# Kernel optimization log

Hardware: AMD Instinct MI355X
Metric: run time of the kernel (lower is better)

Reference implementation:

```python
import jax, jax.numpy as jnp
import numpy as np

HEADS = 8
DIM_HEAD = 64
NUM_PATHWAYS = 281
SCALE = DIM_HEAD ** -0.5


def setup_inputs() -> dict:
    key = jax.random.key(0)
    k1, k2 = jax.random.split(key)
    b, n, dim = 4, 12281, 512  # n = 281 pathway tokens + 12000 histology patch tokens
    x = jax.random.normal(k1, (b, n, dim), dtype=jnp.float32)
    W_qkv = jax.random.normal(k2, (dim, 3 * HEADS * DIM_HEAD), dtype=jnp.float32) * 0.02
    return {"x": x, "W_qkv": W_qkv}


def reference(x, W_qkv):
    b, n, _ = x.shape
    h, d, m = HEADS, DIM_HEAD, NUM_PATHWAYS
    qkv = x @ W_qkv  # [b, n, 3*h*d]
    q, k, v = jnp.split(qkv, 3, axis=-1)
    # [b, n, h*d] -> [b, h, n, d]
    to_bhnd = lambda t: t.reshape(b, n, h, d).transpose(0, 2, 1, 3)
    q, k, v = to_bhnd(q), to_bhnd(k), to_bhnd(v)
    q = q * SCALE

    q_path, q_hist = q[:, :, :m], q[:, :, m:]
    k_path, k_hist = k[:, :, :m], k[:, :, m:]
    v_path, v_hist = v[:, :, :m], v[:, :, m:]

    # histology queries attend to pathway keys: [b, h, n_hist, m]
    attn_hist = jax.nn.softmax(jnp.einsum('bhid,bhjd->bhij', q_hist, k_path), axis=-1)
    # pathway queries attend to histology keys: [b, h, m, n_hist]
    attn_path = jax.nn.softmax(jnp.einsum('bhid,bhjd->bhij', q_path, k_hist), axis=-1)

    out_pathways = jnp.einsum('bhij,bhjd->bhid', attn_hist, v_path)   # [b, h, n_hist, d]
    out_histology = jnp.einsum('bhij,bhjd->bhid', attn_path, v_hist)  # [b, h, m, d]

    cross_token = jnp.concatenate([out_pathways, out_histology], axis=2)  # [b, h, n, d]
    return cross_token.transpose(0, 2, 1, 3).reshape(b, n, h * d)
```

## Files before the change

### kernel.cpp

```cpp
#include <hip/hip_runtime.h>
#include <hip/hip_bf16.h>

#define BATCH  4
#define NTOK   12281
#define DIMIN  512
#define HEADS  8
#define DHEAD  64
#define MPATH  281
#define NHIST  12000
#define QKVC   1536
#define QSCALE 0.125f
#define ROWS   (BATCH * NTOK)
#define MPAD   49152
#define NSPLIT 8
#define KSPL   1504
#define PROWS  320
#define HROWS  12032
#define M1B    576
#define M0B    3000

typedef __attribute__((ext_vector_type(8)))  short        short8v;
typedef __attribute__((ext_vector_type(4)))  float        f32x4;
typedef __attribute__((ext_vector_type(16))) float        f32x16;
typedef __attribute__((ext_vector_type(4)))  unsigned int uint4v;

__device__ __forceinline__ unsigned short f2bf(float f) {
    unsigned x = __builtin_bit_cast(unsigned, f);
    return (unsigned short)((x + 0x7fffu + ((x >> 16) & 1u)) >> 16);
}
__device__ __forceinline__ unsigned pk2(float a, float b) {
    return (unsigned)f2bf(a) | ((unsigned)f2bf(b) << 16);
}
__device__ __forceinline__ unsigned pk2n(float a, float b) {
    unsigned r;
    asm("v_cvt_pk_bf16_f32 %0, %1, %2" : "=v"(r) : "v"(a), "v"(b));
    return r;
}
__device__ __forceinline__ void plswap(unsigned &a, unsigned &b) {
    asm("v_permlane32_swap_b32 %0, %1" : "+v"(a), "+v"(b));
}
__device__ __forceinline__ short8v ld8(const unsigned short* p) {
    return *reinterpret_cast<const short8v*>(p);
}
__device__ __forceinline__ f32x16 MFMA32(short8v a, short8v b, f32x16 c) {
    return __builtin_amdgcn_mfma_f32_32x32x16_bf16(a, b, c, 0, 0, 0);
}
__device__ __forceinline__ void gl16(const char* g, char* l) {
    __builtin_amdgcn_global_load_lds(
        (const __attribute__((address_space(1))) unsigned int*)g,
        (__attribute__((address_space(3))) unsigned int*)l, 16, 0, 0);
}

__global__ __launch_bounds__(256)
void convert_x(const float* __restrict__ x, unsigned short* __restrict__ xb)
{
    size_t i = ((size_t)blockIdx.x * 256 + threadIdx.x) * 8;
    if (i >= (size_t)MPAD * DIMIN) return;
    uint4v o;
    if (i < (size_t)ROWS * DIMIN) {
        float4 a = *reinterpret_cast<const float4*>(x + i);
        float4 b = *reinterpret_cast<const float4*>(x + i + 4);
        o[0] = pk2(a.x, a.y); o[1] = pk2(a.z, a.w);
        o[2] = pk2(b.x, b.y); o[3] = pk2(b.z, b.w);
    } else {
        o[0] = o[1] = o[2] = o[3] = 0u;
    }
    *reinterpret_cast<uint4v*>(xb + i) = o;
}

__global__ __launch_bounds__(256)
void wt_convert(const float* __restrict__ w, unsigned short* __restrict__ wt)
{
    __shared__ unsigned short Ls[64][72];
    const int k0 = blockIdx.x * 64;
    const int n0 = blockIdx.y * 64;
    const int t  = threadIdx.x;
    const int lr = t >> 2;
    const int c0 = (t & 3) * 16;

    const float* sp = w + (size_t)(k0 + lr) * QKVC + n0 + c0;
    #pragma unroll
    for (int j = 0; j < 16; j += 4) {
        float4 a = *reinterpret_cast<const float4*>(sp + j);
        Ls[lr][c0 + j + 0] = f2bf(a.x);
        Ls[lr][c0 + j + 1] = f2bf(a.y);
        Ls[lr][c0 + j + 2] = f2bf(a.z);
        Ls[lr][c0 + j + 3] = f2bf(a.w);
    }
    __syncthreads();

    alignas(16) unsigned short tmp[16];
    #pragma unroll
    for (int j = 0; j < 16; ++j) tmp[j] = Ls[c0 + j][lr];
    unsigned short* dp = wt + (size_t)(n0 + lr) * DIMIN + k0 + c0;
    *reinterpret_cast<short8v*>(dp)     = *reinterpret_cast<short8v*>(&tmp[0]);
    *reinterpret_cast<short8v*>(dp + 8) = *reinterpret_cast<short8v*>(&tmp[8]);
}

__global__ __launch_bounds__(256)
void pad_fill(unsigned short* kpth, unsigned short* vpth,
              unsigned short* khst, unsigned short* vhst)
{
    int i = blockIdx.x * 256 + threadIdx.x;
    const int PPAD = (PROWS - MPATH) * DHEAD;
    const int HPAD = (HROWS - NHIST) * DHEAD;
    if (i < 32 * PPAD) {
        int bh = i / PPAD, r = i - bh * PPAD;
        size_t off = ((size_t)bh * PROWS + MPATH) * DHEAD + r;
        kpth[off] = 0; vpth[off] = 0;
    }
    if (i < 32 * HPAD) {
        int bh = i / HPAD, r = i - bh * HPAD;
        size_t off = ((size_t)bh * HROWS + NHIST) * DHEAD + r;
        khst[off] = 0; vhst[off] = 0;
    }
}

__global__ __launch_bounds__(256, 2)
void qkv_mfma(const unsigned short* __restrict__ xb, const unsigned short* __restrict__ wt,
              unsigned short* __restrict__ qb,
              unsigned short* __restrict__ kpth, unsigned short* __restrict__ khst,
              unsigned short* __restrict__ vpth, unsigned short* __restrict__ vhst)
{
    __shared__ char lds[65536];
    const int tid  = threadIdx.x;
    const int lane = tid & 63;
    const int wid  = tid >> 6;
    const int wr   = wid >> 1;
    const int wc   = wid & 1;

    int id  = blockIdx.x;
    int wg  = (id & 7) * 576 + (id >> 3);
    const int mt = wg / 12, nt = wg - mt * 12;
    const int bm = mt * 128, bn = nt * 128;

    const int arow0 = tid >> 3;
    const int acolS = ((tid & 7) << 4) ^ ((arow0 & 7) << 4);
    const char* xsrc = (const char*)xb + (((size_t)(bm + arow0)) << 10) + acolS;
    const char* wsrc = (const char*)wt + (((size_t)(bn + arow0)) << 10) + acolS;
    char* ldsA = lds + wid * 1024;
    char* ldsB = lds + 16384 + wid * 1024;

    const int rA   = wr * 64 + (lane & 15);
    const int rB   = wc * 64 + (lane & 15);
    const int hi16 = (lane >> 4) << 4;
    const int sxA  = (rA & 7) << 4;
    const int sxB  = (rB & 7) << 4;

    f32x4 acc[4][4];
    #pragma unroll
    for (int m = 0; m < 4; ++m)
        #pragma unroll
        for (int n = 0; n < 4; ++n)
            #pragma unroll
            for (int r = 0; r < 4; ++r) acc[m][n][r] = 0.f;

    auto STAGE = [&](int bufofs, int ks) {
        const char* xs = xsrc + (size_t)ks * 128;
        const char* ws = wsrc + (size_t)ks * 128;
        #pragma unroll
        for (int i = 0; i < 4; ++i)
            gl16(xs + ((size_t)i << 15), ldsA + bufofs + i * 4096);
        #pragma unroll
        for (int i = 0; i < 4; ++i)
            gl16(ws + ((size_t)i << 15), ldsB + bufofs + i * 4096);
    };

    STAGE(0, 0);
    asm volatile("s_waitcnt vmcnt(0)" ::: "memory");
    __syncthreads();

    for (int ks = 0; ks < 8; ++ks) {
        const int cur = ks & 1;
        if (ks < 7) STAGE((cur ^ 1) * 32768, ks + 1);

        const char* A = lds + cur * 32768;
        const char* B = A + 16384;
        #pragma unroll
        for (int kk = 0; kk < 2; ++kk) {
            short8v a[4], b[4];
            #pragma unroll
            for (int m = 0; m < 4; ++m)
                a[m] = *reinterpret_cast<const short8v*>(
                    A + (rA + m * 16) * 128 + ((kk * 64 + hi16) ^ sxA));
            #pragma unroll
            for (int n = 0; n < 4; ++n)
                b[n] = *reinterpret_cast<const short8v*>(
                    B + (rB + n * 16) * 128 + ((kk * 64 + hi16) ^ sxB));
            #pragma unroll
            for (int m = 0; m < 4; ++m)
                #pragma unroll
                for (int n = 0; n < 4; ++n)
                    acc[m][n] = __builtin_amdgcn_mfma_f32_16x16x32_bf16(
                        a[m], b[n], acc[m][n], 0, 0, 0);
        }
        asm volatile("s_waitcnt vmcnt(0)" ::: "memory");
        __syncthreads();
    }

    unsigned short* cl = reinterpret_cast<unsigned short*>(lds);
    const int crow0 = (lane >> 4) * 4;
    const int ccol  = lane & 15;
    #pragma unroll
    for (int n = 0; n < 4; ++n) {
        const int gcb = bn + wc * 64 + n * 16;
        const float scl = (gcb < 512) ? QSCALE : 1.f;
        #pragma unroll
        for (int m = 0; m < 4; ++m) {
            #pragma unroll
            for (int r = 0; r < 4; ++r) {
                int row = wr * 64 + m * 16 + crow0 + r;
                int col = wc * 64 + n * 16 + ccol;
                cl[row * 136 + col] = f2bf(acc[m][n][r] * scl);
            }
        }
    }
    __syncthreads();

    #pragma unroll
    for (int i = 0; i < 8; ++i) {
        const int chunk = tid + i * 256;
        const int row = chunk >> 4;
        const int c8  = (chunk & 15) * 8;
        const int grow = bm + row;
        if (grow < ROWS) {
            uint4v val = *reinterpret_cast<const uint4v*>(cl + row * 136 + c8);
            const int gcol  = bn + c8;
            const int which = gcol >> 9;
            const int rem   = gcol & 511;
            const int hh = rem >> 6, dd = rem & 63;
            const int bb = grow / NTOK;
            const int nn = grow - bb * NTOK;
            const int bh = bb * HEADS + hh;
            unsigned short* dst;
            if (which == 0) {
                dst = qb + ((size_t)bh * NTOK + nn) * DHEAD + dd;
            } else if (which == 1) {
                dst = (nn < MPATH) ? kpth + ((size_t)bh * PROWS + nn) * DHEAD + dd
                                   : khst + ((size_t)bh * HROWS + (nn - MPATH)) * DHEAD + dd;
            } else {
                dst = (nn < MPATH) ? vpth + ((size_t)bh * PROWS + nn) * DHEAD + dd
                                   : vhst + ((size_t)bh * HROWS + (nn - MPATH)) * DHEAD + dd;
            }
            *reinterpret_cast<uint4v*>(dst) = val;
        }
    }
}

__global__ __launch_bounds__(256)
void transpose64(const unsigned short* __restrict__ src, unsigned short* __restrict__ dst,
                 int nrpad)
{
    __shared__ unsigned short Ls[64][72];
    const int bh = blockIdx.y;
    const int r0 = blockIdx.x * 64;
    const unsigned short* s = src + (size_t)bh * nrpad * DHEAD;
    unsigned short*       d = dst + (size_t)bh * nrpad * DHEAD;

    const int t  = threadIdx.x;
    const int lr = t >> 2;
    const int c0 = (t & 3) * 16;

    const unsigned short* sp = s + (size_t)(r0 + lr) * DHEAD + c0;
    *reinterpret_cast<short8v*>(&Ls[lr][c0])     = *reinterpret_cast<const short8v*>(sp);
    *reinterpret_cast<short8v*>(&Ls[lr][c0 + 8]) = *reinterpret_cast<const short8v*>(sp + 8);
    __syncthreads();

    alignas(16) unsigned short tmp[16];
    #pragma unroll
    for (int j = 0; j < 16; ++j) tmp[j] = Ls[c0 + j][lr];
    const int T  = (r0 + c0) >> 5;
    const int kk = (r0 + c0) & 31;
    unsigned short* dp = d + (((size_t)T * 64 + lr) << 5) + kk;
    *reinterpret_cast<short8v*>(dp)     = *reinterpret_cast<short8v*>(&tmp[0]);
    *reinterpret_cast<short8v*>(dp + 8) = *reinterpret_cast<short8v*>(&tmp[8]);
}

__global__ __launch_bounds__(256, 4)
void fused_attn(const unsigned short* __restrict__ qb,
                const unsigned short* __restrict__ kpth, const unsigned short* __restrict__ khst,
                const unsigned short* __restrict__ vtp,  const unsigned short* __restrict__ vth,
                float* __restrict__ out,
                float* __restrict__ pl, float* __restrict__ po)
{
    const int wave = threadIdx.x >> 6;
    const int lane = threadIdx.x & 63;
    const int hi   = lane >> 5;
    const int ql   = lane & 31;

    int bh, qt, sp = 0;
    bool mode0;
    if (blockIdx.x < M1B) {
        mode0 = false;
        const int xcd = blockIdx.x & 7;
        const int i1  = (blockIdx.x >> 3) * 4 + wave;
        bh = i1 / 9;  qt = i1 - bh * 9;  sp = xcd;
    } else {
        mode0 = true;
        const int b0  = blockIdx.x - M1B;
        const int xcd = b0 & 7;
        const int i0  = (b0 >> 3) * 4 + wave;
        const int g   = i0 / 375;
        bh = xcd + 8 * g;  qt = i0 - g * 375;
    }

    const int q0 = mode0 ? (MPATH + qt * 32) : (qt * 32);
    const unsigned short* qrow = qb + ((size_t)bh * NTOK + (q0 + ql)) * DHEAD + hi * 8;
    short8v qf0 = ld8(qrow);
    short8v qf1 = ld8(qrow + 16);
    short8v qf2 = ld8(qrow + 32);
    short8v qf3 = ld8(qrow + 48);

    const unsigned short* kb;
    const unsigned short* vptr;
    int ntiles;
    if (mode0) {
        kb   = kpth + (size_t)bh * PROWS * DHEAD;
        vptr = vtp  + (size_t)bh * PROWS * DHEAD + ql * 32 + hi * 8;
        ntiles = 9;
    } else {
        kb   = khst + ((size_t)bh * HROWS + (size_t)sp * KSPL) * DHEAD;
        vptr = vth  + (size_t)bh * HROWS * DHEAD + (size_t)sp * 47 * 2048 + ql * 32 + hi * 8;
        ntiles = (sp == NSPLIT - 1) ? 46 : 47;
    }
    const unsigned short* kr = kb + (size_t)ql * DHEAD + hi * 8;

    f32x16 o0, o1;
    #pragma unroll
    for (int r = 0; r < 16; ++r) { o0[r] = 0.f; o1[r] = 0.f; }
    float l_loc = 0.f;

    short8v kf0 = ld8(kr);
    short8v kf1 = ld8(kr + 16);
    short8v kf2 = ld8(kr + 32);
    short8v kf3 = ld8(kr + 48);

    for (int t = 0; t < ntiles; ++t) {
        short8v vf0 = ld8(vptr);
        short8v vf1 = ld8(vptr + 16);
        short8v vf2 = ld8(vptr + 1024);
        short8v vf3 = ld8(vptr + 1024 + 16);
        vptr += 2048;

        f32x16 s;
        #pragma unroll
        for (int r = 0; r < 16; ++r) s[r] = 0.f;
        __builtin_amdgcn_s_setprio(1);
        s = MFMA32(kf0, qf0, s);
        s = MFMA32(kf1, qf1, s);
        s = MFMA32(kf2, qf2, s);
        s = MFMA32(kf3, qf3, s);
        __builtin_amdgcn_s_setprio(0);

        if (t + 1 < ntiles) {
            const unsigned short* kn = kr + (size_t)(t + 1) * 32 * DHEAD;
            kf0 = ld8(kn);
            kf1 = ld8(kn + 16);
            kf2 = ld8(kn + 32);
            kf3 = ld8(kn + 48);
        }

        float p[16]; float psum = 0.f;
        if (mode0 && t == 8) {
            #pragma unroll
            for (int r = 0; r < 16; ++r) {
                int krow = (r & 3) + 8 * (r >> 2) + 4 * hi;
                p[r] = (256 + krow >= MPATH) ? 0.f : __expf(s[r]);
                psum += p[r];
            }
        } else {
            #pragma unroll
            for (int r = 0; r < 16; ++r) { p[r] = __expf(s[r]); psum += p[r]; }
        }
        l_loc += psum;

        unsigned G[8];
        #pragma unroll
        for (int g = 0; g < 4; ++g) {
            G[2 * g]     = pk2n(p[4 * g],     p[4 * g + 1]);
            G[2 * g + 1] = pk2n(p[4 * g + 2], p[4 * g + 3]);
        }
        plswap(G[0], G[2]);
        plswap(G[1], G[3]);
        plswap(G[4], G[6]);
        plswap(G[5], G[7]);
        uint4v w0, w1;
        w0[0] = G[0]; w0[1] = G[1]; w0[2] = G[2]; w0[3] = G[3];
        w1[0] = G[4]; w1[1] = G[5]; w1[2] = G[6]; w1[3] = G[7];
        short8v pa0 = __builtin_bit_cast(short8v, w0);
        short8v pa1 = __builtin_bit_cast(short8v, w1);

        __builtin_amdgcn_s_setprio(1);
        o0 = MFMA32(pa0, vf0, o0);
        o0 = MFMA32(pa1, vf1, o0);
        o1 = MFMA32(pa0, vf2, o1);
        o1 = MFMA32(pa1, vf3, o1);
        __builtin_amdgcn_s_setprio(0);
    }

    const float l_run = l_loc + __shfl_xor(l_loc, 32);

    if (mode0) {
        const int bb = bh >> 3, hh = bh & 7;
        float linv = 1.0f / l_run;
        #pragma unroll
        for (int r = 0; r < 16; ++r) {
            int row = (r & 3) + 8 * (r >> 2) + 4 * hi;
            float invr = __shfl(linv, row);
            float* op = out + ((size_t)bb * NTOK + (qt * 32 + row)) * (HEADS * DHEAD) + hh * DHEAD;
            op[ql]      = o0[r] * invr;
            op[32 + ql] = o1[r] * invr;
        }
    } else {
        const size_t pbase = ((size_t)bh * NSPLIT + sp) * MPATH;
        if (hi == 0 && q0 + ql < MPATH)
            pl[pbase + q0 + ql] = l_run;
        #pragma unroll
        for (int r = 0; r < 16; ++r) {
            int row = (r & 3) + 8 * (r >> 2) + 4 * hi;
            int qq = q0 + row;
            if (qq < MPATH) {
                float* pp = po + (pbase + qq) * DHEAD;
                pp[ql]      = o0[r];
                pp[32 + ql] = o1[r];
            }
        }
    }
}

__global__ __launch_bounds__(256)
void combine_kernel(const float* __restrict__ pl, const float* __restrict__ po,
                    float* __restrict__ out)
{
    const int idx = blockIdx.x * 256 + threadIdx.x;
    const int dd  = idx & 63;
    const int r   = idx >> 6;
    if (r >= BATCH * HEADS * MPATH) return;
    const int bh = r / MPATH;
    const int jq = r - bh * MPATH;

    const size_t pbase = ((size_t)bh * NSPLIT) * MPATH + jq;
    float L = 0.f, acc = 0.f;
    #pragma unroll
    for (int s = 0; s < NSPLIT; ++s) {
        L   += pl[pbase + (size_t)s * MPATH];
        acc += po[(pbase + (size_t)s * MPATH) * DHEAD + dd];
    }
    const int bb = bh >> 3, hh = bh & 7;
    out[((size_t)bb * NTOK + (NHIST + jq)) * (HEADS * DHEAD) + hh * DHEAD + dd] = acc / L;
}

extern "C" void kernel_launch(void* const* d_in, const int* in_sizes, int n_in,
                              void* d_out, int out_size, void* d_ws, size_t ws_size,
                              hipStream_t stream)
{
    (void)in_sizes; (void)n_in; (void)out_size; (void)ws_size;
    const float* x = (const float*)d_in[0];
    const float* w = (const float*)d_in[1];
    float* out = (float*)d_out;

    const size_t QEL = (size_t)32 * NTOK * DHEAD;
    const size_t PEL = (size_t)32 * PROWS * DHEAD;
    const size_t HEL = (size_t)32 * HROWS * DHEAD;

    unsigned short* qb   = (unsigned short*)d_ws;
    unsigned short* kpth = qb   + QEL;
    unsigned short* khst = kpth + PEL;
    unsigned short* vpth = khst + HEL;
    unsigned short* vhst = vpth + PEL;
    unsigned short* vtp  = vhst + HEL;
    unsigned short* vth  = vtp  + PEL;
    unsigned short* xb   = vth  + HEL;
    unsigned short* wtb  = xb   + (size_t)MPAD * DIMIN;
    float* pl = (float*)(wtb + (size_t)QKVC * DIMIN);
    float* po = pl + (size_t)32 * NSPLIT * MPATH;

    convert_x<<<(MPAD * DIMIN / 8 + 255) / 256, 256, 0, stream>>>(x, xb);
    wt_convert<<<dim3(DIMIN / 64, QKVC / 64), 256, 0, stream>>>(w, wtb);
    pad_fill<<<312, 256, 0, stream>>>(kpth, vpth, khst, vhst);

    qkv_mfma<<<(MPAD / 128) * (QKVC / 128), 256, 0, stream>>>(xb, wtb, qb,
                                                              kpth, khst, vpth, vhst);

    transpose64<<<dim3(PROWS / 64, 32), 256, 0, stream>>>(vpth, vtp, PROWS);
    transpose64<<<dim3(HROWS / 64, 32), 256, 0, stream>>>(vhst, vth, HROWS);

    fused_attn<<<M1B + M0B, 256, 0, stream>>>(qb, kpth, khst, vtp, vth, out, pl, po);

    const int rows = BATCH * HEADS * MPATH;
    combine_kernel<<<(rows * DHEAD + 255) / 256, 256, 0, stream>>>(pl, po, out);
}
```

Measured before the change: 326.4 us.

## Software-pipeline QK^T one tile ahead and switch softmax to native exp2

The attention loop now computes the score MFMAs for tile t+1 before doing the exponentials and PV MFMAs for tile t, using two ping-pong score accumulators. K loads are prefetched two tiles ahead and V loads one tile ahead. The aim is to overlap the dependent MFMA, exp and pack chain across iterations and hide load latency. The exp is replaced by the hardware exp2, with log2(e) folded into the Q scale constant. This raises register pressure from the second 16-float accumulator and the extra in-flight fragments, which could reduce occupancy.

```diff
diff --git a/kernel.cpp b/kernel.cpp
--- a/kernel.cpp
+++ b/kernel.cpp
@@ -9,7 +9,7 @@
 #define MPATH  281
 #define NHIST  12000
 #define QKVC   1536
-#define QSCALE 0.125f
+#define QSCALE 0.180336884f
 #define ROWS   (BATCH * NTOK)
 #define MPAD   49152
 #define NSPLIT 8
@@ -38,6 +38,9 @@
 }
 __device__ __forceinline__ void plswap(unsigned &a, unsigned &b) {
     asm("v_permlane32_swap_b32 %0, %1" : "+v"(a), "+v"(b));
+}
+__device__ __forceinline__ float fexp2(float x) {
+    return __builtin_amdgcn_exp2f(x);
 }
 __device__ __forceinline__ short8v ld8(const unsigned short* p) {
     return *reinterpret_cast<const short8v*>(p);
@@ -311,19 +314,18 @@
     short8v qf2 = ld8(qrow + 32);
     short8v qf3 = ld8(qrow + 48);
 
-    const unsigned short* kb;
-    const unsigned short* vptr;
+    const unsigned short* kr;
+    const unsigned short* vb;
     int ntiles;
     if (mode0) {
-        kb   = kpth + (size_t)bh * PROWS * DHEAD;
-        vptr = vtp  + (size_t)bh * PROWS * DHEAD + ql * 32 + hi * 8;
+        kr = kpth + (size_t)bh * PROWS * DHEAD + ql * DHEAD + hi * 8;
+        vb = vtp  + (size_t)bh * PROWS * DHEAD + ql * 32 + hi * 8;
         ntiles = 9;
     } else {
-        kb   = khst + ((size_t)bh * HROWS + (size_t)sp * KSPL) * DHEAD;
-        vptr = vth  + (size_t)bh * HROWS * DHEAD + (size_t)sp * 47 * 2048 + ql * 32 + hi * 8;
+        kr = khst + ((size_t)bh * HROWS + (size_t)sp * KSPL) * DHEAD + ql * DHEAD + hi * 8;
+        vb = vth  + (size_t)bh * HROWS * DHEAD + (size_t)sp * 47 * 2048 + ql * 32 + hi * 8;
         ntiles = (sp == NSPLIT - 1) ? 46 : 47;
     }
-    const unsigned short* kr = kb + (size_t)ql * DHEAD + hi * 8;
 
     f32x16 o0, o1;
     #pragma unroll
@@ -334,51 +336,64 @@
     short8v kf1 = ld8(kr + 16);
     short8v kf2 = ld8(kr + 32);
     short8v kf3 = ld8(kr + 48);
-
-    for (int t = 0; t < ntiles; ++t) {
-        short8v vf0 = ld8(vptr);
-        short8v vf1 = ld8(vptr + 16);
-        short8v vf2 = ld8(vptr + 1024);
-        short8v vf3 = ld8(vptr + 1024 + 16);
-        vptr += 2048;
-
-        f32x16 s;
-        #pragma unroll
-        for (int r = 0; r < 16; ++r) s[r] = 0.f;
-        __builtin_amdgcn_s_setprio(1);
-        s = MFMA32(kf0, qf0, s);
-        s = MFMA32(kf1, qf1, s);
-        s = MFMA32(kf2, qf2, s);
-        s = MFMA32(kf3, qf3, s);
-        __builtin_amdgcn_s_setprio(0);
-
-        if (t + 1 < ntiles) {
-            const unsigned short* kn = kr + (size_t)(t + 1) * 32 * DHEAD;
-            kf0 = ld8(kn);
-            kf1 = ld8(kn + 16);
-            kf2 = ld8(kn + 32);
-            kf3 = ld8(kn + 48);
-        }
-
-        float p[16]; float psum = 0.f;
+    short8v vf0 = ld8(vb);
+    short8v vf1 = ld8(vb + 16);
+    short8v vf2 = ld8(vb + 1024);
+    short8v vf3 = ld8(vb + 1040);
+
+    f32x16 sA, sB;
+    #pragma unroll
+    for (int r = 0; r < 16; ++r) sA[r] = 0.f;
+    sA = MFMA32(kf0, qf0, sA);
+    sA = MFMA32(kf1, qf1, sA);
+    sA = MFMA32(kf2, qf2, sA);
+    sA = MFMA32(kf3, qf3, sA);
+    kf0 = ld8(kr + 2048);
+    kf1 = ld8(kr + 2048 + 16);
+    kf2 = ld8(kr + 2048 + 32);
+    kf3 = ld8(kr + 2048 + 48);
+
+    auto body = [&](f32x16& scur, f32x16& snxt, int t) {
+        const bool hn = (t + 1 < ntiles);
+        if (hn) {
+            #pragma unroll
+            for (int r = 0; r < 16; ++r) snxt[r] = 0.f;
+            __builtin_amdgcn_s_setprio(1);
+            snxt = MFMA32(kf0, qf0, snxt);
+            snxt = MFMA32(kf1, qf1, snxt);
+            snxt = MFMA32(kf2, qf2, snxt);
+            snxt = MFMA32(kf3, qf3, snxt);
+            __builtin_amdgcn_s_setprio(0);
+            if (t + 2 < ntiles) {
+                const unsigned short* kn = kr + (size_t)(t + 2) * 2048;
+                kf0 = ld8(kn);
+                kf1 = ld8(kn + 16);
+                kf2 = ld8(kn + 32);
+                kf3 = ld8(kn + 48);
+            }
+        }
+        float psum = 0.f;
         if (mode0 && t == 8) {
             #pragma unroll
             for (int r = 0; r < 16; ++r) {
                 int krow = (r & 3) + 8 * (r >> 2) + 4 * hi;
-                p[r] = (256 + krow >= MPATH) ? 0.f : __expf(s[r]);
-                psum += p[r];
+                float e = (256 + krow >= MPATH) ? 0.f : fexp2(scur[r]);
+                scur[r] = e; psum += e;
             }
         } else {
             #pragma unroll
-            for (int r = 0; r < 16; ++r) { p[r] = __expf(s[r]); psum += p[r]; }
+            for (int r = 0; r < 16; ++r) {
+                float e = fexp2(scur[r]);
+                scur[r] = e; psum += e;
+            }
         }
         l_loc += psum;
 
         unsigned G[8];
         #pragma unroll
         for (int g = 0; g < 4; ++g) {
-            G[2 * g]     = pk2n(p[4 * g],     p[4 * g + 1]);
-            G[2 * g + 1] = pk2n(p[4 * g + 2], p[4 * g + 3]);
+            G[2 * g]     = pk2n(scur[4 * g],     scur[4 * g + 1]);
+            G[2 * g + 1] = pk2n(scur[4 * g + 2], scur[4 * g + 3]);
         }
         plswap(G[0], G[2]);
         plswap(G[1], G[3]);
@@ -396,6 +411,21 @@
         o1 = MFMA32(pa0, vf2, o1);
         o1 = MFMA32(pa1, vf3, o1);
         __builtin_amdgcn_s_setprio(0);
+
+        if (hn) {
+            const unsigned short* vn = vb + (size_t)(t + 1) * 2048;
+            vf0 = ld8(vn);
+            vf1 = ld8(vn + 16);
+            vf2 = ld8(vn + 1024);
+            vf3 = ld8(vn + 1040);
+        }
+    };
+
+    for (int t = 0;;) {
+        body(sA, sB, t);
+        if (++t >= ntiles) break;
+        body(sB, sA, t);
+        if (++t >= ntiles) break;
     }
 
     const float l_run = l_loc + __shfl_xor(l_loc, 32);
```

Measured after the change: 594.1 us. 82.0% more time.

## Process two query tiles per wave, use exp2 with folded log2e scale, split keys 16 ways

Applied to the files above, without the earlier changes.

Each wave now handles 64 queries (two 32-row tiles) and reuses every loaded K and V fragment across both, which halves K/V load traffic per query. The Q scale folds in log2(e) so the softmax can call the hardware exp2 directly instead of __expf. The histology-key split grows from 8 to 16 chunks, with new grid sizes, and the launch bound drops to 2 blocks per SIMD to leave room for the extra accumulators. The Q buffer gets padding so the over-read of the last tile stays in bounds. Costs include higher register pressure, lower occupancy, more partial results for the combine step, and some idle waves (pw>=5 return early).

```diff
diff --git a/kernel.cpp b/kernel.cpp
--- a/kernel.cpp
+++ b/kernel.cpp
@@ -9,15 +9,16 @@
 #define MPATH  281
 #define NHIST  12000
 #define QKVC   1536
-#define QSCALE 0.125f
+#define QSCALE 0.180336884f
 #define ROWS   (BATCH * NTOK)
 #define MPAD   49152
-#define NSPLIT 8
-#define KSPL   1504
+#define NSPLIT 16
+#define KSPL   768
 #define PROWS  320
 #define HROWS  12032
-#define M1B    576
-#define M0B    3000
+#define M1B    1024
+#define M0B    1504
+#define QPAD   4096
 
 typedef __attribute__((ext_vector_type(8)))  short        short8v;
 typedef __attribute__((ext_vector_type(4)))  float        f32x4;
@@ -38,6 +39,9 @@
 }
 __device__ __forceinline__ void plswap(unsigned &a, unsigned &b) {
     asm("v_permlane32_swap_b32 %0, %1" : "+v"(a), "+v"(b));
+}
+__device__ __forceinline__ float fexp2(float x) {
+    return __builtin_amdgcn_exp2f(x);
 }
 __device__ __forceinline__ short8v ld8(const unsigned short* p) {
     return *reinterpret_cast<const short8v*>(p);
@@ -276,8 +280,8 @@
     *reinterpret_cast<short8v*>(dp + 8) = *reinterpret_cast<short8v*>(&tmp[8]);
 }
 
-__global__ __launch_bounds__(256, 4)
-void fused_attn(const unsigned short* __restrict__ qb,
+__global__ __launch_bounds__(256, 2)
+void fused_attn(const unsigned short* __restrict__ qbuf,
                 const unsigned short* __restrict__ kpth, const unsigned short* __restrict__ khst,
                 const unsigned short* __restrict__ vtp,  const unsigned short* __restrict__ vth,
                 float* __restrict__ out,
@@ -288,141 +292,175 @@
     const int hi   = lane >> 5;
     const int ql   = lane & 31;
 
-    int bh, qt, sp = 0;
+    int bh, pw, sp = 0;
     bool mode0;
     if (blockIdx.x < M1B) {
         mode0 = false;
         const int xcd = blockIdx.x & 7;
-        const int i1  = (blockIdx.x >> 3) * 4 + wave;
-        bh = i1 / 9;  qt = i1 - bh * 9;  sp = xcd;
+        const int jj  = blockIdx.x >> 3;
+        bh = jj >> 2;
+        const int rem = jj & 3;
+        sp = xcd + 8 * (rem & 1);
+        pw = (rem >> 1) * 4 + wave;
+        if (pw >= 5) return;
     } else {
         mode0 = true;
         const int b0  = blockIdx.x - M1B;
         const int xcd = b0 & 7;
-        const int i0  = (b0 >> 3) * 4 + wave;
-        const int g   = i0 / 375;
-        bh = xcd + 8 * g;  qt = i0 - g * 375;
-    }
-
-    const int q0 = mode0 ? (MPATH + qt * 32) : (qt * 32);
-    const unsigned short* qrow = qb + ((size_t)bh * NTOK + (q0 + ql)) * DHEAD + hi * 8;
-    short8v qf0 = ld8(qrow);
-    short8v qf1 = ld8(qrow + 16);
-    short8v qf2 = ld8(qrow + 32);
-    short8v qf3 = ld8(qrow + 48);
-
-    const unsigned short* kb;
-    const unsigned short* vptr;
+        const int i   = b0 >> 3;
+        const int g   = i / 47;
+        bh = xcd + 8 * g;
+        pw = (i - g * 47) * 4 + wave;
+    }
+
+    const int q0 = mode0 ? (MPATH + pw * 64) : (pw * 64);
+    const unsigned short* qra = qbuf + ((size_t)bh * NTOK + (q0 + ql)) * DHEAD + hi * 8;
+    const unsigned short* qrb = qra + (size_t)32 * DHEAD;
+    short8v qA0 = ld8(qra),      qA1 = ld8(qra + 16);
+    short8v qA2 = ld8(qra + 32), qA3 = ld8(qra + 48);
+    short8v qB0 = ld8(qrb),      qB1 = ld8(qrb + 16);
+    short8v qB2 = ld8(qrb + 32), qB3 = ld8(qrb + 48);
+
+    const unsigned short* kr;
+    const unsigned short* vb;
     int ntiles;
     if (mode0) {
-        kb   = kpth + (size_t)bh * PROWS * DHEAD;
-        vptr = vtp  + (size_t)bh * PROWS * DHEAD + ql * 32 + hi * 8;
+        kr = kpth + (size_t)bh * PROWS * DHEAD + ql * DHEAD + hi * 8;
+        vb = vtp  + (size_t)bh * PROWS * DHEAD + ql * 32 + hi * 8;
         ntiles = 9;
     } else {
-        kb   = khst + ((size_t)bh * HROWS + (size_t)sp * KSPL) * DHEAD;
-        vptr = vth  + (size_t)bh * HROWS * DHEAD + (size_t)sp * 47 * 2048 + ql * 32 + hi * 8;
-        ntiles = (sp == NSPLIT - 1) ? 46 : 47;
-    }
-    const unsigned short* kr = kb + (size_t)ql * DHEAD + hi * 8;
-
-    f32x16 o0, o1;
-    #pragma unroll
-    for (int r = 0; r < 16; ++r) { o0[r] = 0.f; o1[r] = 0.f; }
-    float l_loc = 0.f;
-
-    short8v kf0 = ld8(kr);
-    short8v kf1 = ld8(kr + 16);
-    short8v kf2 = ld8(kr + 32);
-    short8v kf3 = ld8(kr + 48);
+        kr = khst + ((size_t)bh * HROWS + (size_t)sp * KSPL) * DHEAD + ql * DHEAD + hi * 8;
+        vb = vth  + (size_t)bh * HROWS * DHEAD + (size_t)sp * 24 * 2048 + ql * 32 + hi * 8;
+        ntiles = (sp == NSPLIT - 1) ? 15 : 24;
+    }
+
+    f32x16 o0, o1, o2, o3, SZ;
+    #pragma unroll
+    for (int r = 0; r < 16; ++r) { o0[r] = 0.f; o1[r] = 0.f; o2[r] = 0.f; o3[r] = 0.f; SZ[r] = 0.f; }
+    float lA = 0.f, lB = 0.f;
+
+    short8v kf0 = ld8(kr), kf1 = ld8(kr + 16), kf2 = ld8(kr + 32), kf3 = ld8(kr + 48);
 
     for (int t = 0; t < ntiles; ++t) {
-        short8v vf0 = ld8(vptr);
-        short8v vf1 = ld8(vptr + 16);
-        short8v vf2 = ld8(vptr + 1024);
-        short8v vf3 = ld8(vptr + 1024 + 16);
-        vptr += 2048;
-
-        f32x16 s;
-        #pragma unroll
-        for (int r = 0; r < 16; ++r) s[r] = 0.f;
+        const unsigned short* vp = vb + (size_t)t * 2048;
+        short8v vf0 = ld8(vp);
+        short8v vf1 = ld8(vp + 16);
+        short8v vf2 = ld8(vp + 1024);
+        short8v vf3 = ld8(vp + 1040);
+
         __builtin_amdgcn_s_setprio(1);
-        s = MFMA32(kf0, qf0, s);
-        s = MFMA32(kf1, qf1, s);
-        s = MFMA32(kf2, qf2, s);
-        s = MFMA32(kf3, qf3, s);
+        f32x16 sA = MFMA32(kf0, qA0, SZ);
+        sA = MFMA32(kf1, qA1, sA);
+        sA = MFMA32(kf2, qA2, sA);
+        sA = MFMA32(kf3, qA3, sA);
+        f32x16 sB = MFMA32(kf0, qB0, SZ);
+        sB = MFMA32(kf1, qB1, sB);
+        sB = MFMA32(kf2, qB2, sB);
+        sB = MFMA32(kf3, qB3, sB);
         __builtin_amdgcn_s_setprio(0);
 
         if (t + 1 < ntiles) {
-            const unsigned short* kn = kr + (size_t)(t + 1) * 32 * DHEAD;
-            kf0 = ld8(kn);
-            kf1 = ld8(kn + 16);
-            kf2 = ld8(kn + 32);
-            kf3 = ld8(kn + 48);
-        }
-
-        float p[16]; float psum = 0.f;
+            const unsigned short* kn = kr + (size_t)(t + 1) * 2048;
+            kf0 = ld8(kn);      kf1 = ld8(kn + 16);
+            kf2 = ld8(kn + 32); kf3 = ld8(kn + 48);
+        }
+
+        float psA = 0.f, psB = 0.f;
         if (mode0 && t == 8) {
             #pragma unroll
             for (int r = 0; r < 16; ++r) {
                 int krow = (r & 3) + 8 * (r >> 2) + 4 * hi;
-                p[r] = (256 + krow >= MPATH) ? 0.f : __expf(s[r]);
-                psum += p[r];
+                float eA = (256 + krow >= MPATH) ? 0.f : fexp2(sA[r]);
+                float eB = (256 + krow >= MPATH) ? 0.f : fexp2(sB[r]);
+                sA[r] = eA; psA += eA;
+                sB[r] = eB; psB += eB;
             }
         } else {
             #pragma unroll
-            for (int r = 0; r < 16; ++r) { p[r] = __expf(s[r]); psum += p[r]; }
-        }
-        l_loc += psum;
-
-        unsigned G[8];
-        #pragma unroll
-        for (int g = 0; g < 4; ++g) {
-            G[2 * g]     = pk2n(p[4 * g],     p[4 * g + 1]);
-            G[2 * g + 1] = pk2n(p[4 * g + 2], p[4 * g + 3]);
-        }
-        plswap(G[0], G[2]);
-        plswap(G[1], G[3]);
-        plswap(G[4], G[6]);
-        plswap(G[5], G[7]);
-        uint4v w0, w1;
-        w0[0] = G[0]; w0[1] = G[1]; w0[2] = G[2]; w0[3] = G[3];
-        w1[0] = G[4]; w1[1] = G[5]; w1[2] = G[6]; w1[3] = G[7];
-        short8v pa0 = __builtin_bit_cast(short8v, w0);
-        short8v pa1 = __builtin_bit_cast(short8v, w1);
+            for (int r = 0; r < 16; ++r) {
+                float eA = fexp2(sA[r]); sA[r] = eA; psA += eA;
+                float eB = fexp2(sB[r]); sB[r] = eB; psB += eB;
+            }
+        }
+        lA += psA; lB += psB;
+
+        unsigned A0 = pk2n(sA[0],  sA[1]),  A1 = pk2n(sA[2],  sA[3]);
+        unsigned A2 = pk2n(sA[4],  sA[5]),  A3 = pk2n(sA[6],  sA[7]);
+        unsigned A4 = pk2n(sA[8],  sA[9]),  A5 = pk2n(sA[10], sA[11]);
+        unsigned A6 = pk2n(sA[12], sA[13]), A7 = pk2n(sA[14], sA[15]);
+        plswap(A0, A2); plswap(A1, A3); plswap(A4, A6); plswap(A5, A7);
+        uint4v wA0, wA1;
+        wA0[0] = A0; wA0[1] = A1; wA0[2] = A2; wA0[3] = A3;
+        wA1[0] = A4; wA1[1] = A5; wA1[2] = A6; wA1[3] = A7;
+        short8v paA0 = __builtin_bit_cast(short8v, wA0);
+        short8v paA1 = __builtin_bit_cast(short8v, wA1);
+        unsigned B0 = pk2n(sB[0],  sB[1]),  B1 = pk2n(sB[2],  sB[3]);
+        unsigned B2 = pk2n(sB[4],  sB[5]),  B3 = pk2n(sB[6],  sB[7]);
+        unsigned B4 = pk2n(sB[8],  sB[9]),  B5 = pk2n(sB[10], sB[11]);
+        unsigned B6 = pk2n(sB[12], sB[13]), B7 = pk2n(sB[14], sB[15]);
+        plswap(B0, B2); plswap(B1, B3); plswap(B4, B6); plswap(B5, B7);
+        uint4v wB0, wB1;
+        wB0[0] = B0; wB0[1] = B1; wB0[2] = B2; wB0[3] = B3;
+        wB1[0] = B4; wB1[1] = B5; wB1[2] = B6; wB1[3] = B7;
+        short8v paB0 = __builtin_bit_cast(short8v, wB0);
+        short8v paB1 = __builtin_bit_cast(short8v, wB1);
 
         __builtin_amdgcn_s_setprio(1);
-        o0 = MFMA32(pa0, vf0, o0);
-        o0 = MFMA32(pa1, vf1, o0);
-        o1 = MFMA32(pa0, vf2, o1);
-        o1 = MFMA32(pa1, vf3, o1);
+        o0 = MFMA32(paA0, vf0, o0);
+        o0 = MFMA32(paA1, vf1, o0);
+        o1 = MFMA32(paA0, vf2, o1);
+        o1 = MFMA32(paA1, vf3, o1);
+        o2 = MFMA32(paB0, vf0, o2);
+        o2 = MFMA32(paB1, vf1, o2);
+        o3 = MFMA32(paB0, vf2, o3);
+        o3 = MFMA32(paB1, vf3, o3);
         __builtin_amdgcn_s_setprio(0);
     }
 
-    const float l_run = l_loc + __shfl_xor(l_loc, 32);
+    const float lAr = lA + __shfl_xor(lA, 32);
+    const float lBr = lB + __shfl_xor(lB, 32);
 
     if (mode0) {
         const int bb = bh >> 3, hh = bh & 7;
-        float linv = 1.0f / l_run;
+        const float liA = 1.0f / lAr;
+        const float liB = 1.0f / lBr;
         #pragma unroll
         for (int r = 0; r < 16; ++r) {
-            int row = (r & 3) + 8 * (r >> 2) + 4 * hi;
-            float invr = __shfl(linv, row);
-            float* op = out + ((size_t)bb * NTOK + (qt * 32 + row)) * (HEADS * DHEAD) + hh * DHEAD;
-            op[ql]      = o0[r] * invr;
-            op[32 + ql] = o1[r] * invr;
+            const int row = (r & 3) + 8 * (r >> 2) + 4 * hi;
+            {
+                float invr = __shfl(liA, row);
+                float* op = out + ((size_t)bb * NTOK + (pw * 64 + row)) * (HEADS * DHEAD) + hh * DHEAD;
+                op[ql]      = o0[r] * invr;
+                op[32 + ql] = o1[r] * invr;
+            }
+            const int tokB = pw * 64 + 32 + row;
+            if (tokB < NHIST) {
+                float invr = __shfl(liB, row);
+                float* op = out + ((size_t)bb * NTOK + tokB) * (HEADS * DHEAD) + hh * DHEAD;
+                op[ql]      = o2[r] * invr;
+                op[32 + ql] = o3[r] * invr;
+            }
         }
     } else {
         const size_t pbase = ((size_t)bh * NSPLIT + sp) * MPATH;
-        if (hi == 0 && q0 + ql < MPATH)
-            pl[pbase + q0 + ql] = l_run;
+        if (hi == 0) {
+            if (q0 + ql < MPATH)      pl[pbase + q0 + ql]      = lAr;
+            if (q0 + 32 + ql < MPATH) pl[pbase + q0 + 32 + ql] = lBr;
+        }
         #pragma unroll
         for (int r = 0; r < 16; ++r) {
-            int row = (r & 3) + 8 * (r >> 2) + 4 * hi;
-            int qq = q0 + row;
-            if (qq < MPATH) {
-                float* pp = po + (pbase + qq) * DHEAD;
+            const int row = (r & 3) + 8 * (r >> 2) + 4 * hi;
+            const int qqA = q0 + row;
+            if (qqA < MPATH) {
+                float* pp = po + (pbase + qqA) * DHEAD;
                 pp[ql]      = o0[r];
                 pp[32 + ql] = o1[r];
+            }
+            const int qqB = q0 + 32 + row;
+            if (qqB < MPATH) {
+                float* pp = po + (pbase + qqB) * DHEAD;
+                pp[ql]      = o2[r];
+                pp[32 + ql] = o3[r];
             }
         }
     }
@@ -459,7 +497,7 @@
     const float* w = (const float*)d_in[1];
     float* out = (float*)d_out;
 
-    const size_t QEL = (size_t)32 * NTOK * DHEAD;
+    const size_t QEL = (size_t)32 * NTOK * DHEAD + QPAD;
     const size_t PEL = (size_t)32 * PROWS * DHEAD;
     const size_t HEL = (size_t)32 * HROWS * DHEAD;
 
```

Result: faster. 296.6 us (-9.1%).
